# Optimization experiments

Measured on AMD Instinct MI355X. Metric: run time of the kernel, lower is better.

Reference implementation:

```python
import jax, jax.numpy as jnp
import numpy as np

B, S, D, H = 4, 2048, 1024, 16
DH = D // H
MAX_SEQ = 2048
OUT = 1024


def setup_inputs() -> dict:
    key = jax.random.key(0)
    ks = jax.random.split(key, 10)
    inp = {
        "x": jax.random.normal(ks[0], (B, S, D), dtype=jnp.float32),
        "src_key_padding_mask": jnp.ones((B, S), dtype=jnp.float32),  # 1 = valid token
        "pos_emb": jax.random.normal(ks[1], (1, MAX_SEQ, D), dtype=jnp.float32),
        "ln_gamma": jnp.ones((D,), dtype=jnp.float32),
        "ln_beta": jnp.zeros((D,), dtype=jnp.float32),
        "in_proj_weight": jax.random.normal(ks[2], (3 * D, D), dtype=jnp.float32) * (1.0 / np.sqrt(D)),
        "in_proj_bias": jnp.zeros((3 * D,), dtype=jnp.float32),
        "out_proj_weight": jax.random.normal(ks[3], (D, D), dtype=jnp.float32) * (1.0 / np.sqrt(D)),
        "out_proj_bias": jnp.zeros((D,), dtype=jnp.float32),
        "to_out_weight": jax.random.normal(ks[4], (OUT, D), dtype=jnp.float32) * (1.0 / np.sqrt(D)),
        "to_out_bias": jnp.zeros((OUT,), dtype=jnp.float32),
    }
    return inp


def _layernorm(x, gamma, beta, eps=1e-5):
    mu = jnp.mean(x, axis=-1, keepdims=True)
    var = jnp.mean(jnp.square(x - mu), axis=-1, keepdims=True)
    return (x - mu) * jax.lax.rsqrt(var + eps) * gamma + beta


def reference(x, src_key_padding_mask, pos_emb, ln_gamma, ln_beta,
              in_proj_weight, in_proj_bias, out_proj_weight, out_proj_bias,
              to_out_weight, to_out_bias):
    seq = x.shape[1]
    xn = _layernorm(x, ln_gamma, ln_beta)
    xp = xn + pos_emb[:, :seq, :]  # [B,S,D]

    # PyTorch quirk: 1.0 - mask.long() is a FLOAT tensor -> treated as ADDITIVE mask.
    add_mask = (1.0 - src_key_padding_mask)[:, None, None, :]  # [B,1,1,S]

    qkv = xp @ in_proj_weight.T + in_proj_bias  # [B,S,3D]
    q, k, v = jnp.split(qkv, 3, axis=-1)
    # [B,H,S,DH]
    q = q.reshape(B, seq, H, DH).transpose(0, 2, 1, 3)
    k = k.reshape(B, seq, H, DH).transpose(0, 2, 1, 3)
    v = v.reshape(B, seq, H, DH).transpose(0, 2, 1, 3)

    scores = jnp.einsum("bhqd,bhkd->bhqk", q, k) / jnp.sqrt(jnp.float32(DH))
    scores = scores + add_mask
    attn = jax.nn.softmax(scores, axis=-1)
    o = jnp.einsum("bhqk,bhkd->bhqd", attn, v)  # [B,H,S,DH]
    o = o.transpose(0, 2, 1, 3).reshape(B, seq, D)
    attn_out = o @ out_proj_weight.T + out_proj_bias

    return (xp + attn_out) @ to_out_weight.T + to_out_bias
```

## Files before the change

### kernel.cpp

```cpp
#include <hip/hip_runtime.h>
#include <stdint.h>
#include <stddef.h>

typedef unsigned short u16;
typedef __bf16 bf16x8 __attribute__((ext_vector_type(8)));
typedef float floatx4 __attribute__((ext_vector_type(4)));

#define B_  4
#define S_  2048
#define D_  1024
#define H_  16
#define DH_ 64

__device__ __forceinline__ float b2f(u16 u) {
  union { unsigned u; float f; } c; c.u = ((unsigned)u) << 16; return c.f;
}
__device__ __forceinline__ u16 f2b(float f) {
  union { float f; unsigned u; } c; c.f = f;
  unsigned u = c.u;
  u += 0x7fffu + ((u >> 16) & 1u);
  return (u16)(u >> 16);
}

__device__ __forceinline__ void gld_lds16(const u16* g, u16* l) {
  __builtin_amdgcn_global_load_lds(
      (const __attribute__((address_space(1))) unsigned int*)g,
      (__attribute__((address_space(3))) unsigned int*)l, 16, 0, 0);
}

__device__ __forceinline__ unsigned cvtpk(float lo, float hi) {
  unsigned r;
  asm("v_cvt_pk_bf16_f32 %0, %1, %2" : "=v"(r) : "v"(lo), "v"(hi));
  return r;
}

#define PL32(a, b) asm("v_permlane32_swap_b32 %0, %1" : "+v"(a), "+v"(b))
#define PL16(a, b) asm("v_permlane16_swap_b32 %0, %1" : "+v"(a), "+v"(b))

union B8 { unsigned u[4]; bf16x8 v; };

__global__ __launch_bounds__(256) void cvt_f32_bf16(
    const float* __restrict__ src, u16* __restrict__ dst, int n)
{
  int i = (blockIdx.x * 256 + threadIdx.x) * 4;
  if (i >= n) return;
  float4 v = *(const float4*)(src + i);
  u16 o[4] __attribute__((aligned(8)));
  o[0] = f2b(v.x); o[1] = f2b(v.y); o[2] = f2b(v.z); o[3] = f2b(v.w);
  *(uint2*)(dst + i) = *(uint2*)o;
}

__global__ __launch_bounds__(256) void ln_pos_kernel(
    const float* __restrict__ x, const float* __restrict__ pos,
    const float* __restrict__ gamma, const float* __restrict__ beta,
    u16* __restrict__ xp)
{
  const int row = blockIdx.x;
  const int s = row & (S_ - 1);
  const int t = threadIdx.x;
  const int lane = t & 63, w = t >> 6;

  float4 xv = *(const float4*)(x + (size_t)row * D_ + t * 4);
  float f[4] = {xv.x, xv.y, xv.z, xv.w};
  float sum = f[0] + f[1] + f[2] + f[3];
  float sq  = f[0]*f[0] + f[1]*f[1] + f[2]*f[2] + f[3]*f[3];
#pragma unroll
  for (int m = 1; m < 64; m <<= 1) {
    sum += __shfl_xor(sum, m);
    sq  += __shfl_xor(sq, m);
  }
  __shared__ float red[8];
  if (lane == 0) { red[w] = sum; red[4 + w] = sq; }
  __syncthreads();
  sum = red[0] + red[1] + red[2] + red[3];
  sq  = red[4] + red[5] + red[6] + red[7];
  const float mu = sum * (1.f / D_);
  const float rstd = rsqrtf(fmaxf(sq * (1.f / D_) - mu * mu, 0.f) + 1e-5f);

  float4 gv = *(const float4*)(gamma + t * 4);
  float4 bv = *(const float4*)(beta + t * 4);
  float4 pv = *(const float4*)(pos + (size_t)s * D_ + t * 4);
  float g[4] = {gv.x, gv.y, gv.z, gv.w};
  float bb[4] = {bv.x, bv.y, bv.z, bv.w};
  float pp[4] = {pv.x, pv.y, pv.z, pv.w};
  u16 ov[4] __attribute__((aligned(8)));
#pragma unroll
  for (int i = 0; i < 4; ++i)
    ov[i] = f2b((f[i] - mu) * rstd * g[i] + bb[i] + pp[i]);
  *(uint2*)(xp + (size_t)row * D_ + t * 4) = *(uint2*)ov;
}

template<int HAS_BIAS, int HAS_RES, int OUT_F32>
__global__ __launch_bounds__(256) void gemm_bt(
    const u16* A, const u16* __restrict__ Bm,
    const float* __restrict__ bias, const u16* res,
    void* Cv, int M, int N, int K, int lda, int ldc)
{
  __shared__ u16 As[128 * 32];
  __shared__ u16 Bs[128 * 32];
  const int tid = threadIdx.x;
  const int lane = tid & 63, w = tid >> 6;
  const int quad = lane >> 4, l4 = lane & 15;
  const int wm = (w >> 1) * 64, wn = (w & 1) * 64;
  const int m0 = blockIdx.y * 128, n0 = blockIdx.x * 128;

  const u16* Ag = A + (size_t)m0 * lda;
  const u16* Bg = Bm + (size_t)n0 * K;

  const int s0 = tid, s1 = tid + 256;
  const int r0 = s0 >> 2, c0 = ((s0 & 3) - (r0 >> 1)) & 3;
  const int r1 = s1 >> 2, c1 = ((s1 & 3) - (r1 >> 1)) & 3;
  const int pA = (quad + (l4 >> 1)) & 3;

  floatx4 acc[4][4] = {};

  for (int k0 = 0; k0 < K; k0 += 32) {
    __syncthreads();
    gld_lds16(Ag + (size_t)r0 * lda + k0 + c0 * 8, &As[s0 * 8]);
    gld_lds16(Ag + (size_t)r1 * lda + k0 + c1 * 8, &As[s1 * 8]);
    gld_lds16(Bg + (size_t)r0 * K + k0 + c0 * 8, &Bs[s0 * 8]);
    gld_lds16(Bg + (size_t)r1 * K + k0 + c1 * 8, &Bs[s1 * 8]);
    __syncthreads();
    bf16x8 af[4], bfr[4];
#pragma unroll
    for (int i = 0; i < 4; ++i)
      af[i] = *(const bf16x8*)&As[(wm + i * 16 + l4) * 32 + pA * 8];
#pragma unroll
    for (int j = 0; j < 4; ++j)
      bfr[j] = *(const bf16x8*)&Bs[(wn + j * 16 + l4) * 32 + pA * 8];
#pragma unroll
    for (int i = 0; i < 4; ++i)
#pragma unroll
      for (int j = 0; j < 4; ++j)
        acc[i][j] = __builtin_amdgcn_mfma_f32_16x16x32_bf16(af[i], bfr[j], acc[i][j], 0, 0, 0);
  }

#pragma unroll
  for (int i = 0; i < 4; ++i) {
#pragma unroll
    for (int j = 0; j < 4; ++j) {
      const int col = n0 + wn + j * 16 + l4;
      float bvv = 0.f;
      if (HAS_BIAS) bvv = bias[col];
#pragma unroll
      for (int r = 0; r < 4; ++r) {
        const int row = m0 + wm + i * 16 + quad * 4 + r;
        float v = acc[i][j][r] + bvv;
        if (HAS_RES) v += b2f(res[(size_t)row * ldc + col]);
        v = fminf(fmaxf(v, -60000.f), 60000.f);
        if (OUT_F32) ((float*)Cv)[(size_t)row * ldc + col] = v;
        else         ((u16*)Cv)[(size_t)row * ldc + col] = f2b(v);
      }
    }
  }
}

__global__ __launch_bounds__(256, 4) void attn_kernel(
    u16* qkv, const float* __restrict__ mask)
{
  __shared__ u16 Ks[128 * 64];
  __shared__ u16 Vt[64 * 136];

  const int tid = threadIdx.x;
  const int lane = tid & 63, w = tid >> 6;
  const int quad = lane >> 4, l4 = lane & 15;
  const int qb = blockIdx.x;
  const int bh = blockIdx.y;
  const int b = bh >> 4, h = bh & 15;
  const int q0 = qb * 64;

  const size_t rstr = 3 * D_;
  u16* qbase = qkv + (size_t)b * S_ * rstr + h * DH_;

  bf16x8 qfrag[2];
  {
    const u16* qp = qbase + (size_t)(q0 + w * 16 + l4) * rstr + quad * 8;
    qfrag[0] = *(const bf16x8*)(qp);
    qfrag[1] = *(const bf16x8*)(qp + 32);
  }

  floatx4 acc_o[4] = {};
  float l_run = 0.f;

  for (int j = 0; j < 16; ++j) {
    __syncthreads();
    const u16* kbase = qkv + ((size_t)b * S_ + j * 128) * rstr + D_ + h * DH_;
#pragma unroll
    for (int t = 0; t < 4; ++t) {
      int sidx = tid + t * 256;
      int rr = sidx >> 3, ch = ((sidx & 7) - rr) & 7;
      gld_lds16(kbase + (size_t)rr * rstr + ch * 8, &Ks[sidx * 8]);
    }
    {
      const u16* vbase = qkv + ((size_t)b * S_ + j * 128) * rstr + 2 * D_ + h * DH_;
      int s = tid & 127, d0 = (tid >> 7) * 32;
      const u16* vp = vbase + (size_t)s * rstr + d0;
      u16 v[32] __attribute__((aligned(16)));
      *(uint4*)(v)      = *(const uint4*)(vp);
      *(uint4*)(v + 8)  = *(const uint4*)(vp + 8);
      *(uint4*)(v + 16) = *(const uint4*)(vp + 16);
      *(uint4*)(v + 24) = *(const uint4*)(vp + 24);
#pragma unroll
      for (int d = 0; d < 32; ++d) Vt[(d0 + d) * 136 + s] = v[d];
    }
    __syncthreads();

    floatx4 accs[8] = {};
#pragma unroll
    for (int kc = 0; kc < 2; ++kc)
#pragma unroll
      for (int tj = 0; tj < 8; ++tj) {
        const int rk = tj * 16 + l4;
        bf16x8 kf = *(const bf16x8*)&Ks[rk * 64 + (((kc * 4 + quad) + rk) & 7) * 8];
        accs[tj] = __builtin_amdgcn_mfma_f32_16x16x32_bf16(kf, qfrag[kc], accs[tj], 0, 0, 0);
      }

    const float* mrow = mask + (size_t)b * S_ + j * 128 + quad * 4;
    float rsum = 0.f;
    unsigned pk[8][2];
#pragma unroll
    for (int tj = 0; tj < 8; ++tj) {
      float4 mv = *(const float4*)(mrow + tj * 16);
      float p0 = __expf(fminf(fmaf(accs[tj][0], 0.125f, 1.0f - mv.x), 30.f));
      float p1 = __expf(fminf(fmaf(accs[tj][1], 0.125f, 1.0f - mv.y), 30.f));
      float p2 = __expf(fminf(fmaf(accs[tj][2], 0.125f, 1.0f - mv.z), 30.f));
      float p3 = __expf(fminf(fmaf(accs[tj][3], 0.125f, 1.0f - mv.w), 30.f));
      rsum += (p0 + p1) + (p2 + p3);
      pk[tj][0] = cvtpk(p0, p1);
      pk[tj][1] = cvtpk(p2, p3);
    }
    rsum += __shfl_xor(rsum, 16);
    rsum += __shfl_xor(rsum, 32);
    l_run += rsum;

#pragma unroll
    for (int kc = 0; kc < 4; ++kc) {
      unsigned x0 = pk[2 * kc][0], x1 = pk[2 * kc + 1][0];
      unsigned y0 = pk[2 * kc][1], y1 = pk[2 * kc + 1][1];
      PL32(x0, x1); PL32(y0, y1);
      PL16(x0, x1); PL16(y0, y1);
      B8 pa; pa.u[0] = x0; pa.u[1] = y0; pa.u[2] = x1; pa.u[3] = y1;
      __builtin_amdgcn_s_setprio(1);
#pragma unroll
      for (int tn = 0; tn < 4; ++tn) {
        bf16x8 bfr = *(const bf16x8*)&Vt[(tn * 16 + l4) * 136 + kc * 32 + quad * 8];
        acc_o[tn] = __builtin_amdgcn_mfma_f32_16x16x32_bf16(pa.v, bfr, acc_o[tn], 0, 0, 0);
      }
      __builtin_amdgcn_s_setprio(0);
    }
  }

  float inv[4];
#pragma unroll
  for (int r = 0; r < 4; ++r) inv[r] = 1.0f / __shfl(l_run, quad * 4 + r);
#pragma unroll
  for (int tn = 0; tn < 4; ++tn) {
#pragma unroll
    for (int r = 0; r < 4; ++r) {
      const int row = q0 + w * 16 + quad * 4 + r;
      const int col = h * DH_ + tn * 16 + l4;
      qkv[((size_t)b * S_ + row) * rstr + col] = f2b(acc_o[tn][r] * inv[r]);
    }
  }
}

extern "C" void kernel_launch(void* const* d_in, const int* in_sizes, int n_in,
                              void* d_out, int out_size, void* d_ws, size_t ws_size,
                              hipStream_t stream) {
  const float* x    = (const float*)d_in[0];
  const float* mask = (const float*)d_in[1];
  const float* pos  = (const float*)d_in[2];
  const float* gam  = (const float*)d_in[3];
  const float* bet  = (const float*)d_in[4];
  const float* wqkv = (const float*)d_in[5];
  const float* bqkv = (const float*)d_in[6];
  const float* wo   = (const float*)d_in[7];
  const float* bo   = (const float*)d_in[8];
  const float* wt   = (const float*)d_in[9];
  const float* bt   = (const float*)d_in[10];
  float* out = (float*)d_out;

  char* ws = (char*)d_ws;
  u16* qkvb = (u16*)(ws);
  u16* xp   = (u16*)(ws + (size_t)50331648);

  u16* wqkv_b = (u16*)d_out;
  u16* wo_b   = (u16*)((char*)d_out + (size_t)6291456);
  u16* wt_b   = qkvb;

  const int nqkv = 3 * D_ * D_;
  const int nd   = D_ * D_;

  cvt_f32_bf16<<<nqkv / 1024, 256, 0, stream>>>(wqkv, wqkv_b, nqkv);
  cvt_f32_bf16<<<nd   / 1024, 256, 0, stream>>>(wo,   wo_b,   nd);
  ln_pos_kernel<<<B_ * S_, 256, 0, stream>>>(x, pos, gam, bet, xp);
  gemm_bt<1, 0, 0><<<dim3(3 * D_ / 128, B_ * S_ / 128), 256, 0, stream>>>(
      xp, wqkv_b, bqkv, nullptr, qkvb, B_ * S_, 3 * D_, D_, D_, 3 * D_);
  attn_kernel<<<dim3(S_ / 64, B_ * H_), 256, 0, stream>>>(qkvb, mask);
  gemm_bt<1, 1, 0><<<dim3(D_ / 128, B_ * S_ / 128), 256, 0, stream>>>(
      qkvb, wo_b, bo, xp, xp, B_ * S_, D_, D_, 3 * D_, D_);
  cvt_f32_bf16<<<nd / 1024, 256, 0, stream>>>(wt, wt_b, nd);
  gemm_bt<1, 0, 1><<<dim3(D_ / 128, B_ * S_ / 128), 256, 0, stream>>>(
      xp, wt_b, bt, nullptr, out, B_ * S_, D_, D_, D_, D_);
}
```

Measured before the change: 415.5 us.

## Double-buffer K/V tiles in attention with 64-key blocks and prefetch

Shrinks the attention key block from 128 to 64 and double-buffers K and transposed V in shared memory. The next tile's K is loaded asynchronously and its V is held in registers while the current tile is computed, so global-load latency overlaps with MFMA work and one barrier per iteration is removed. In exchange there are twice as many iterations with smaller MFMA batches between barriers, and more register pressure from the V prefetch.

Result: slower. 424.4 us (+2.2%).

```diff
diff --git a/kernel.cpp b/kernel.cpp
--- a/kernel.cpp
+++ b/kernel.cpp
@@ -158,8 +158,8 @@
 __global__ __launch_bounds__(256, 4) void attn_kernel(
     u16* qkv, const float* __restrict__ mask)
 {
-  __shared__ u16 Ks[128 * 64];
-  __shared__ u16 Vt[64 * 136];
+  __shared__ u16 Ks[2][64 * 64];
+  __shared__ u16 Vt[2][64 * 72];
 
   const int tid = threadIdx.x;
   const int lane = tid & 63, w = tid >> 6;
@@ -179,47 +179,61 @@
     qfrag[1] = *(const bf16x8*)(qp + 32);
   }
 
+  const u16* kbase0 = qkv + (size_t)b * S_ * rstr + D_ + h * DH_;
+  const u16* vbase0 = kbase0 + D_;
+  const int vs = tid & 63, vd0 = (tid >> 6) * 16;
+
   floatx4 acc_o[4] = {};
   float l_run = 0.f;
-
-  for (int j = 0; j < 16; ++j) {
-    __syncthreads();
-    const u16* kbase = qkv + ((size_t)b * S_ + j * 128) * rstr + D_ + h * DH_;
-#pragma unroll
-    for (int t = 0; t < 4; ++t) {
+  u16 vreg[16] __attribute__((aligned(16)));
+
+  {
+    const u16* kb = kbase0;
+#pragma unroll
+    for (int t = 0; t < 2; ++t) {
       int sidx = tid + t * 256;
       int rr = sidx >> 3, ch = ((sidx & 7) - rr) & 7;
-      gld_lds16(kbase + (size_t)rr * rstr + ch * 8, &Ks[sidx * 8]);
-    }
-    {
-      const u16* vbase = qkv + ((size_t)b * S_ + j * 128) * rstr + 2 * D_ + h * DH_;
-      int s = tid & 127, d0 = (tid >> 7) * 32;
-      const u16* vp = vbase + (size_t)s * rstr + d0;
-      u16 v[32] __attribute__((aligned(16)));
-      *(uint4*)(v)      = *(const uint4*)(vp);
-      *(uint4*)(v + 8)  = *(const uint4*)(vp + 8);
-      *(uint4*)(v + 16) = *(const uint4*)(vp + 16);
-      *(uint4*)(v + 24) = *(const uint4*)(vp + 24);
-#pragma unroll
-      for (int d = 0; d < 32; ++d) Vt[(d0 + d) * 136 + s] = v[d];
-    }
-    __syncthreads();
-
-    floatx4 accs[8] = {};
+      gld_lds16(kb + (size_t)rr * rstr + ch * 8, &Ks[0][sidx * 8]);
+    }
+    const u16* vp = vbase0 + (size_t)vs * rstr + vd0;
+    *(uint4*)(vreg)     = *(const uint4*)(vp);
+    *(uint4*)(vreg + 8) = *(const uint4*)(vp + 8);
+  }
+  __syncthreads();
+#pragma unroll
+  for (int d = 0; d < 16; ++d) Vt[0][(vd0 + d) * 72 + vs] = vreg[d];
+  __syncthreads();
+
+  int cur = 0;
+  for (int j = 0; j < 32; ++j) {
+    if (j < 31) {
+      const u16* vp = vbase0 + ((size_t)(j + 1) * 64 + vs) * rstr + vd0;
+      *(uint4*)(vreg)     = *(const uint4*)(vp);
+      *(uint4*)(vreg + 8) = *(const uint4*)(vp + 8);
+      const u16* kb = kbase0 + (size_t)(j + 1) * 64 * rstr;
+#pragma unroll
+      for (int t = 0; t < 2; ++t) {
+        int sidx = tid + t * 256;
+        int rr = sidx >> 3, ch = ((sidx & 7) - rr) & 7;
+        gld_lds16(kb + (size_t)rr * rstr + ch * 8, &Ks[cur ^ 1][sidx * 8]);
+      }
+    }
+
+    floatx4 accs[4] = {};
 #pragma unroll
     for (int kc = 0; kc < 2; ++kc)
 #pragma unroll
-      for (int tj = 0; tj < 8; ++tj) {
+      for (int tj = 0; tj < 4; ++tj) {
         const int rk = tj * 16 + l4;
-        bf16x8 kf = *(const bf16x8*)&Ks[rk * 64 + (((kc * 4 + quad) + rk) & 7) * 8];
+        bf16x8 kf = *(const bf16x8*)&Ks[cur][rk * 64 + (((kc * 4 + quad) + rk) & 7) * 8];
         accs[tj] = __builtin_amdgcn_mfma_f32_16x16x32_bf16(kf, qfrag[kc], accs[tj], 0, 0, 0);
       }
 
-    const float* mrow = mask + (size_t)b * S_ + j * 128 + quad * 4;
+    const float* mrow = mask + (size_t)b * S_ + j * 64 + quad * 4;
     float rsum = 0.f;
-    unsigned pk[8][2];
-#pragma unroll
-    for (int tj = 0; tj < 8; ++tj) {
+    unsigned pk[4][2];
+#pragma unroll
+    for (int tj = 0; tj < 4; ++tj) {
       float4 mv = *(const float4*)(mrow + tj * 16);
       float p0 = __expf(fminf(fmaf(accs[tj][0], 0.125f, 1.0f - mv.x), 30.f));
       float p1 = __expf(fminf(fmaf(accs[tj][1], 0.125f, 1.0f - mv.y), 30.f));
@@ -234,7 +248,7 @@
     l_run += rsum;
 
 #pragma unroll
-    for (int kc = 0; kc < 4; ++kc) {
+    for (int kc = 0; kc < 2; ++kc) {
       unsigned x0 = pk[2 * kc][0], x1 = pk[2 * kc + 1][0];
       unsigned y0 = pk[2 * kc][1], y1 = pk[2 * kc + 1][1];
       PL32(x0, x1); PL32(y0, y1);
@@ -243,11 +257,19 @@
       __builtin_amdgcn_s_setprio(1);
 #pragma unroll
       for (int tn = 0; tn < 4; ++tn) {
-        bf16x8 bfr = *(const bf16x8*)&Vt[(tn * 16 + l4) * 136 + kc * 32 + quad * 8];
+        bf16x8 bfr = *(const bf16x8*)&Vt[cur][(tn * 16 + l4) * 72 + kc * 32 + quad * 8];
         acc_o[tn] = __builtin_amdgcn_mfma_f32_16x16x32_bf16(pa.v, bfr, acc_o[tn], 0, 0, 0);
       }
       __builtin_amdgcn_s_setprio(0);
     }
+
+    if (j < 31) {
+#pragma unroll
+      for (int d = 0; d < 16; ++d) Vt[cur ^ 1][(vd0 + d) * 72 + vs] = vreg[d];
+    }
+
+    __syncthreads();
+    cur ^= 1;
   }
 
   float inv[4];
```
